# Optimization experiments

Hardware: AMD Instinct MI355X
Metric: run time of the kernel (lower is better)

Reference implementation:

```python
import jax, jax.numpy as jnp
import numpy as np

B, N, D, H = 16, 512, 256, 8
E_PER = 16384  # edges per graph (avg degree 32)
BN_EPS = 1e-5


def _bn(x, g, b, m, v):
    # BatchNorm1d in eval mode: normalize with running stats
    return (x - m) * (g * jax.lax.rsqrt(v + BN_EPS)) + b


def setup_inputs() -> dict:
    key = jax.random.key(0)
    ks = jax.random.split(key, 32)
    E = B * E_PER
    w = lambda k, s: (jax.random.normal(k, s, jnp.float32) * 0.02)
    # block-diagonal edge list: indices within each graph + graph offset
    src = jax.random.randint(ks[1], (B, E_PER), 0, N)
    dst = jax.random.randint(ks[2], (B, E_PER), 0, N)
    off = (jnp.arange(B) * N)[:, None]
    inp = {
        "x": jax.random.normal(ks[0], (B * N, D), jnp.float32),
        "edge_rows": (src + off).reshape(-1).astype(jnp.int32),
        "edge_cols": (dst + off).reshape(-1).astype(jnp.int32),
        "edge_vals": jax.random.uniform(ks[3], (E,), jnp.float32) * 0.1,
        "w_gcn": w(ks[4], (D, D)),
        "in_proj_w": w(ks[5], (3 * D, D)),
        "in_proj_b": w(ks[6], (3 * D,)),
        "out_proj_w": w(ks[7], (D, D)),
        "out_proj_b": w(ks[8], (D,)),
        "w1": w(ks[9], (4 * D, D)),
        "b1": w(ks[10], (4 * D,)),
        "w2": w(ks[11], (D, 4 * D)),
        "b2": w(ks[12], (D,)),
        "batch_size": B,
        "num_nodes": N,
    }
    for i, name in enumerate(["bn1", "bn2", "bn3"]):
        k4 = jax.random.split(ks[13 + i], 4)
        inp[name + "_g"] = 1.0 + jax.random.uniform(k4[0], (D,), jnp.float32) * 0.1
        inp[name + "_b"] = w(k4[1], (D,))
        inp[name + "_m"] = w(k4[2], (D,))
        inp[name + "_v"] = 1.0 + jax.random.uniform(k4[3], (D,), jnp.float32) * 0.1
    return inp


def reference(x, edge_rows, edge_cols, edge_vals, w_gcn,
              in_proj_w, in_proj_b, out_proj_w, out_proj_b,
              bn1_g, bn1_b, bn1_m, bn1_v,
              bn2_g, bn2_b, bn2_m, bn2_v,
              bn3_g, bn3_b, bn3_m, bn3_v,
              w1, b1, w2, b2, batch_size, num_nodes):
    n_total = x.shape[0]
    dh = D // H
    # --- local GCN: linear -> sparse SpMM (gather/scatter) -> exact GELU ---
    hl = x @ w_gcn.T                                            # (BN, D)
    agg = jax.ops.segment_sum(edge_vals[:, None] * hl[edge_cols],
                              edge_rows, num_segments=n_total)   # (BN, D)
    h_local = jax.nn.gelu(agg, approximate=False)
    x = x + h_local
    x = _bn(x, bn1_g, bn1_b, bn1_m, bn1_v)
    # --- global multi-head self-attention per graph ---
    h = x.reshape(batch_size, num_nodes, D)
    qkv = jnp.einsum('bnd,ed->bne', h, in_proj_w) + in_proj_b    # (B, N, 3D)
    q, k, v = jnp.split(qkv, 3, axis=-1)
    q = q.reshape(batch_size, num_nodes, H, dh)
    k = k.reshape(batch_size, num_nodes, H, dh)
    v = v.reshape(batch_size, num_nodes, H, dh)
    scores = jnp.einsum('bqhd,bkhd->bhqk', q, k) / jnp.sqrt(jnp.float32(dh))
    attn = jax.nn.softmax(scores, axis=-1)
    ctx = jnp.einsum('bhqk,bkhd->bqhd', attn, v).reshape(batch_size, num_nodes, D)
    h_attn = (ctx @ out_proj_w.T + out_proj_b).reshape(n_total, D)
    x = x + h_attn
    x = _bn(x, bn2_g, bn2_b, bn2_m, bn2_v)
    # --- FFN ---
    h_ffn = jax.nn.gelu(x @ w1.T + b1, approximate=False) @ w2.T + b2
    x = x + h_ffn
    x = _bn(x, bn3_g, bn3_b, bn3_m, bn3_v)
    return x
```

## Files before the change

kernel.cpp:

```cpp
#include <hip/hip_runtime.h>
#include <hip/hip_bf16.h>
#include <math.h>

#define D_    256
#define NT_   8192
#define NN_   512
#define B_    16
#define H_    8
#define EPG_  16384
#define BN_EPS 1e-5f

typedef __attribute__((ext_vector_type(8))) short bx8;
typedef __attribute__((ext_vector_type(4))) short sx4;
typedef __attribute__((ext_vector_type(4))) float fx4;

__device__ __forceinline__ float gelu_exact(float x) {
    return 0.5f * x * (1.0f + erff(x * 0.70710678118654752f));
}
__device__ __forceinline__ short bf16s(float v) {
    __hip_bfloat16 hb = __float2bfloat16(v);
    return *(short*)&hb;
}

typedef __attribute__((address_space(1))) const unsigned int GU;
typedef __attribute__((address_space(3))) unsigned int LU;
__device__ __forceinline__ void gl_lds16(const void* g, void* l) {
    __builtin_amdgcn_global_load_lds((GU*)g, (LU*)l, 16, 0, 0);
}

template<int TM, int TN, int EPI, int OBF, int RBF>
__global__ __launch_bounds__(256)
void mgemm(const short* __restrict__ A, const short* __restrict__ Bw,
           const float* __restrict__ bias, void* __restrict__ Cout,
           int M, int N, int K,
           long sA, long sB, long sC, long sR,
           const void* __restrict__ resid,
           const float* __restrict__ bng, const float* __restrict__ bnb,
           const float* __restrict__ bnm, const float* __restrict__ bnv)
{
    constexpr int MR = TM / 32, NR = TN / 32;
    constexpr int NIA = TM / 8, NIB = TN / 8;
    __shared__ short As[2][TM][64];
    __shared__ short Bs[2][TN][64];
    const int bz = blockIdx.z;
    A  += (size_t)bz * sA;
    Bw += (size_t)bz * sB;
    const int bm = blockIdx.y * TM, bn = blockIdx.x * TN;
    const int tid = threadIdx.x;
    const int w = tid >> 6, lane = tid & 63;
    const int wm = w >> 1, wn = w & 1;
    const int fr = lane & 15;
    const int srow = lane >> 3;
    const int scol = (((lane & 7) ^ (srow & 7)) << 3);
    fx4 acc[MR][NR] = {};

    auto STAGE = [&](int buf, int k0) {
        #pragma unroll
        for (int i = w; i < NIA + NIB; i += 4) {
            if (i < NIA)
                gl_lds16(A + (size_t)(bm + i * 8 + srow) * K + k0 + scol,
                         (char*)&As[buf][0][0] + i * 1024);
            else
                gl_lds16(Bw + (size_t)(bn + (i - NIA) * 8 + srow) * K + k0 + scol,
                         (char*)&Bs[buf][0][0] + (i - NIA) * 1024);
        }
    };

    STAGE(0, 0);
    __syncthreads();
    const int T = K >> 6;
    for (int t = 0; t < T; ++t) {
        const int cur = t & 1;
        if (t + 1 < T) STAGE(cur ^ 1, (t + 1) << 6);
        #pragma unroll
        for (int ks = 0; ks < 2; ++ks) {
            const int sl = (ks << 2) | (lane >> 4);
            bx8 af[MR], bf[NR];
            #pragma unroll
            for (int m = 0; m < MR; ++m) {
                const int row = wm * (TM / 2) + m * 16 + fr;
                af[m] = *(const bx8*)&As[cur][row][(sl ^ (row & 7)) << 3];
            }
            #pragma unroll
            for (int n = 0; n < NR; ++n) {
                const int row = wn * (TN / 2) + n * 16 + fr;
                bf[n] = *(const bx8*)&Bs[cur][row][(sl ^ (row & 7)) << 3];
            }
            #pragma unroll
            for (int m = 0; m < MR; ++m)
                #pragma unroll
                for (int n = 0; n < NR; ++n)
                    acc[m][n] = __builtin_amdgcn_mfma_f32_16x16x32_bf16(af[m], bf[n], acc[m][n], 0, 0, 0);
        }
        __syncthreads();
    }

    float* Cf = (float*)Cout + (size_t)bz * sC;
    __hip_bfloat16* Cb = (__hip_bfloat16*)Cout + (size_t)bz * sC;
    const float* Rf = (const float*)resid + ((EPI == 2 || EPI == 3) ? (size_t)bz * sR : 0);
    const __hip_bfloat16* Rb = (const __hip_bfloat16*)resid + ((EPI == 2 || EPI == 3) ? (size_t)bz * sR : 0);
    #pragma unroll
    for (int m = 0; m < MR; ++m) {
        #pragma unroll
        for (int n = 0; n < NR; ++n) {
            const int gm0 = bm + wm * (TM / 2) + m * 16 + (lane >> 4) * 4;
            const int gn  = bn + wn * (TN / 2) + n * 16 + fr;
            float vv[4];
            #pragma unroll
            for (int r = 0; r < 4; ++r) {
                const int gm = gm0 + r;
                float v = acc[m][n][r];
                if (bias) v += bias[gn];
                if (EPI == 1) v = gelu_exact(v);
                if (EPI == 2 || EPI == 3) {
                    const float rv = RBF ? __bfloat162float(Rb[(size_t)gm * N + gn])
                                         : Rf[(size_t)gm * N + gn];
                    if (EPI == 2) v += rv;
                    else          v = rv + gelu_exact(v);
                    v = (v - bnm[gn]) * (bng[gn] * rsqrtf(bnv[gn] + BN_EPS)) + bnb[gn];
                }
                vv[r] = v;
            }
            if (EPI == 4) {
                const int tc = (int)sR;
                if (gn >= tc) {
                    short* Tout = (short*)resid;
                    sx4 pk;
                    #pragma unroll
                    for (int r = 0; r < 4; ++r) pk[r] = bf16s(vv[r]);
                    *(sx4*)(Tout + ((size_t)((gm0 >> 9) * (N - tc) + (gn - tc))) * 512 + (gm0 & 511)) = pk;
                } else {
                    #pragma unroll
                    for (int r = 0; r < 4; ++r)
                        Cb[(size_t)(gm0 + r) * N + gn] = __float2bfloat16(vv[r]);
                }
            } else {
                #pragma unroll
                for (int r = 0; r < 4; ++r) {
                    if (OBF) Cb[(size_t)(gm0 + r) * N + gn] = __float2bfloat16(vv[r]);
                    else     Cf[(size_t)(gm0 + r) * N + gn] = vv[r];
                }
            }
        }
    }
}

__device__ __forceinline__ void cv4(const float4 v, __hip_bfloat16* d) {
    __hip_bfloat162* dp = (__hip_bfloat162*)d;
    dp[0] = __hip_bfloat162(__float2bfloat16(v.x), __float2bfloat16(v.y));
    dp[1] = __hip_bfloat162(__float2bfloat16(v.z), __float2bfloat16(v.w));
}

__global__ __launch_bounds__(256)
void conv6(const float* __restrict__ x,  const float* __restrict__ wg,
           const float* __restrict__ iw, const float* __restrict__ ow,
           const float* __restrict__ w1, const float* __restrict__ w2,
           __hip_bfloat16* xb, __hip_bfloat16* wgb, __hip_bfloat16* iwb,
           __hip_bfloat16* owb, __hip_bfloat16* w1b, __hip_bfloat16* w2b)
{
    int i = blockIdx.x * 256 + threadIdx.x;
    const float* s; __hip_bfloat16* d; int o;
    if      (i < 524288) { s = x;  d = xb;  o = i; }
    else if (i < 540672) { s = wg; d = wgb; o = i - 524288; }
    else if (i < 589824) { s = iw; d = iwb; o = i - 540672; }
    else if (i < 606208) { s = ow; d = owb; o = i - 589824; }
    else if (i < 671744) { s = w1; d = w1b; o = i - 606208; }
    else                 { s = w2; d = w2b; o = i - 671744; }
    cv4(((const float4*)s)[o], d + (size_t)o * 4);
}

__global__ __launch_bounds__(256)
void convA(const float* __restrict__ s, __hip_bfloat16* __restrict__ d, int n4)
{
    int i = blockIdx.x * 256 + threadIdx.x;
    if (i >= n4) return;
    cv4(((const float4*)s)[i], d + (size_t)i * 4);
}

__global__ __launch_bounds__(256)
void build_S(const int* __restrict__ rows, const int* __restrict__ cols,
             const float* __restrict__ vals, float* __restrict__ SA)
{
    const int e = blockIdx.x * 256 + threadIdx.x;
    const int r = rows[e], c = cols[e];
    const int g = r >> 9;
    atomicAdd(&SA[((size_t)g << 18) + (size_t)(r & 511) * 512 + (c - (g << 9))], vals[e]);
}

__global__ __launch_bounds__(256, 1)
void attn_mfma(const short* __restrict__ qkv, const short* __restrict__ VtG,
               __hip_bfloat16* __restrict__ ctx)
{
    const int swz = (blockIdx.x & 7) * 128 + (blockIdx.x >> 3);
    const int qt = swz & 7;
    const int h  = (swz >> 3) & 7;
    const int b  = swz >> 6;
    __shared__ short Ks[512][40];
    __shared__ short Vt[32][520];
    __shared__ short Ps[64][520];
    const int tid = threadIdx.x;
    const int lane = tid & 63, wq = tid >> 6;
    const short* base = qkv + (size_t)b * NN_ * 768;
    const short* vtb  = VtG + (size_t)(b * 8 + h) * 32 * 512;

    {
        const int d0 = (tid & 3) << 3;
        const int k0 = tid >> 2;
        #pragma unroll
        for (int rep = 0; rep < 8; ++rep) {
            const int key = k0 + rep * 64;
            *(bx8*)&Ks[key][d0] =
                *(const bx8*)(base + (size_t)key * 768 + 256 + h * 32 + d0);
        }
    }
    {
        const int d = tid >> 3, c0 = (tid & 7) << 3;
        #pragma unroll
        for (int rep = 0; rep < 8; ++rep) {
            const int c = c0 + rep * 64;
            *(bx8*)&Vt[d][c] = *(const bx8*)(vtb + (size_t)d * 512 + c);
        }
    }
    const int fr = lane & 15, fk = (lane >> 4) << 3;
    const int qrow = qt * 64 + wq * 16 + fr;
    bx8 qf = *(const bx8*)(base + (size_t)qrow * 768 + h * 32 + fk);
    __syncthreads();

    fx4 sc[32];
    #pragma unroll
    for (int nt = 0; nt < 32; ++nt) {
        bx8 kf = *(const bx8*)&Ks[nt * 16 + fr][fk];
        fx4 z = {0.f, 0.f, 0.f, 0.f};
        sc[nt] = __builtin_amdgcn_mfma_f32_16x16x32_bf16(kf, qf, z, 0, 0, 0);
    }

    const float scale = 0.17677669529663687f;
    float mx = -1e30f;
    #pragma unroll
    for (int nt = 0; nt < 32; ++nt)
        mx = fmaxf(mx, fmaxf(fmaxf(sc[nt][0], sc[nt][1]), fmaxf(sc[nt][2], sc[nt][3])));
    mx = fmaxf(mx, __shfl_xor(mx, 16, 64));
    mx = fmaxf(mx, __shfl_xor(mx, 32, 64));
    const float M = mx * scale;
    float s = 0.f;
    #pragma unroll
    for (int nt = 0; nt < 32; ++nt) {
        #pragma unroll
        for (int r = 0; r < 4; ++r) {
            const float p = __expf(sc[nt][r] * scale - M);
            sc[nt][r] = p;
            s += p;
        }
    }
    s += __shfl_xor(s, 16, 64);
    s += __shfl_xor(s, 32, 64);
    const float inv = 1.0f / s;
    {
        const int q = wq * 16 + fr;
        const int kb = (lane >> 4) << 2;
        #pragma unroll
        for (int nt = 0; nt < 32; ++nt) {
            sx4 pk;
            #pragma unroll
            for (int r = 0; r < 4; ++r) pk[r] = bf16s(sc[nt][r] * inv);
            *(sx4*)&Ps[q][nt * 16 + kb] = pk;
        }
    }

    fx4 oacc[2] = {};
    #pragma unroll
    for (int step = 0; step < 16; ++step) {
        bx8 pf = *(const bx8*)&Ps[wq * 16 + fr][step * 32 + fk];
        #pragma unroll
        for (int nt = 0; nt < 2; ++nt) {
            bx8 vf = *(const bx8*)&Vt[nt * 16 + fr][step * 32 + fk];
            oacc[nt] = __builtin_amdgcn_mfma_f32_16x16x32_bf16(pf, vf, oacc[nt], 0, 0, 0);
        }
    }
    #pragma unroll
    for (int nt = 0; nt < 2; ++nt) {
        #pragma unroll
        for (int r = 0; r < 4; ++r) {
            const int q = qt * 64 + wq * 16 + (lane >> 4) * 4 + r;
            const int d = nt * 16 + fr;
            ctx[(size_t)(b * NN_ + q) * D_ + h * 32 + d] = __float2bfloat16(oacc[nt][r]);
        }
    }
}

extern "C" void kernel_launch(void* const* d_in, const int* in_sizes, int n_in,
                              void* d_out, int out_size, void* d_ws, size_t ws_size,
                              hipStream_t stream) {
    const float* x      = (const float*)d_in[0];
    const int*   erows  = (const int*)d_in[1];
    const int*   ecols  = (const int*)d_in[2];
    const float* evals  = (const float*)d_in[3];
    const float* w_gcn  = (const float*)d_in[4];
    const float* in_w   = (const float*)d_in[5];
    const float* in_b   = (const float*)d_in[6];
    const float* outw   = (const float*)d_in[7];
    const float* outb   = (const float*)d_in[8];
    const float* w1     = (const float*)d_in[9];
    const float* b1     = (const float*)d_in[10];
    const float* w2     = (const float*)d_in[11];
    const float* b2     = (const float*)d_in[12];
    const float* bn1g = (const float*)d_in[15], *bn1b = (const float*)d_in[16];
    const float* bn1m = (const float*)d_in[17], *bn1v = (const float*)d_in[18];
    const float* bn2g = (const float*)d_in[19], *bn2b = (const float*)d_in[20];
    const float* bn2m = (const float*)d_in[21], *bn2v = (const float*)d_in[22];
    const float* bn3g = (const float*)d_in[23], *bn3b = (const float*)d_in[24];
    const float* bn3m = (const float*)d_in[25], *bn3v = (const float*)d_in[26];

    short* wsS = (short*)d_ws;
    __hip_bfloat16* xb    = (__hip_bfloat16*)(wsS + 0);
    __hip_bfloat16* wgcnb = (__hip_bfloat16*)(wsS + 2097152);
    __hip_bfloat16* iwb   = (__hip_bfloat16*)(wsS + 2162688);
    __hip_bfloat16* owb   = (__hip_bfloat16*)(wsS + 2359296);
    __hip_bfloat16* w1b   = (__hip_bfloat16*)(wsS + 2424832);
    __hip_bfloat16* w2b   = (__hip_bfloat16*)(wsS + 2686976);
    short* VtG  = wsS + 2949120;
    short* hlB  = wsS + 5046272;
    short* x1b  = wsS + 7143424;
    short* ctxb = wsS + 9240576;
    short* x2b  = wsS + 11337728;
    short* h1b  = wsS + 13434880;
    short* SAb  = wsS + 21823488;
    float* SA   = (float*)(wsS + 26017792);
    short* qkvb = wsS + 26017792;
    float* out  = (float*)d_out;

    dim3 blk(256);
    conv6<<<dim3(2880), blk, 0, stream>>>(x, w_gcn, in_w, outw, w1, w2,
                                          xb, wgcnb, iwb, owb, w1b, w2b);
    hipMemsetAsync(SA, 0, (size_t)16 * 512 * 512 * 4, stream);
    build_S<<<dim3(1024), blk, 0, stream>>>(erows, ecols, evals, SA);
    convA<<<dim3(4096), blk, 0, stream>>>(SA, (__hip_bfloat16*)SAb, 1048576);
    mgemm<64,64,4,1,0><<<dim3(4, 128), blk, 0, stream>>>((const short*)xb, (const short*)wgcnb,
        nullptr, nullptr, NT_, D_, D_, 0,0,0,0, hlB, nullptr, nullptr, nullptr, nullptr);
    mgemm<64,64,3,1,0><<<dim3(4, 8, 16), blk, 0, stream>>>(SAb, hlB, nullptr, x1b,
        512, D_, 512, 262144, 131072, 131072, 131072,
        x, bn1g, bn1b, bn1m, bn1v);
    mgemm<64,64,4,1,0><<<dim3(12, 128), blk, 0, stream>>>(x1b, (const short*)iwb, in_b, qkvb,
        NT_, 3 * D_, D_, 0,0,0,512, VtG, nullptr, nullptr, nullptr, nullptr);
    attn_mfma<<<dim3(1024), blk, 0, stream>>>(qkvb, VtG, (__hip_bfloat16*)ctxb);
    mgemm<64,64,2,1,1><<<dim3(4, 128), blk, 0, stream>>>(ctxb, (const short*)owb, outb, x2b,
        NT_, D_, D_, 0,0,0,0, x1b, bn2g, bn2b, bn2m, bn2v);
    mgemm<64,64,1,1,0><<<dim3(16, 128), blk, 0, stream>>>(x2b, (const short*)w1b, b1, h1b,
        NT_, 4 * D_, D_, 0,0,0,0, nullptr, nullptr, nullptr, nullptr, nullptr);
    mgemm<64,64,2,0,1><<<dim3(4, 128), blk, 0, stream>>>(h1b, (const short*)w2b, b2, out,
        NT_, D_, 4 * D_, 0,0,0,0, x2b, bn3g, bn3b, bn3m, bn3v);
}
```

Measured before the change: 230.6 us.

## Stage full 256-wide K chunks in GEMM; read K/V directly from global in attention

The GEMM drops its double-buffered 64-wide K tiles and loads a whole 256-wide K chunk into LDS per step, with a single sync around each chunk. This cuts the number of barriers and loop iterations but gives up overlap between loads and compute and uses more LDS per block. The attention kernel stops copying K and V^T into shared memory and reads the MFMA fragments straight from global memory. That frees LDS so launch bounds can allow 2 blocks per SM, at the cost of uncoalesced, cache-dependent global reads.

```diff
diff --git a/kernel.cpp b/kernel.cpp
--- a/kernel.cpp
+++ b/kernel.cpp
@@ -39,9 +39,9 @@
            const float* __restrict__ bnm, const float* __restrict__ bnv)
 {
     constexpr int MR = TM / 32, NR = TN / 32;
-    constexpr int NIA = TM / 8, NIB = TN / 8;
-    __shared__ short As[2][TM][64];
-    __shared__ short Bs[2][TN][64];
+    constexpr int NIA = TM / 2, NIB = TN / 2;
+    __shared__ short As[TM][256];
+    __shared__ short Bs[TN][256];
     const int bz = blockIdx.z;
     A  += (size_t)bz * sA;
     Bw += (size_t)bz * sB;
@@ -49,42 +49,44 @@
     const int tid = threadIdx.x;
     const int w = tid >> 6, lane = tid & 63;
     const int wm = w >> 1, wn = w & 1;
-    const int fr = lane & 15;
-    const int srow = lane >> 3;
-    const int scol = (((lane & 7) ^ (srow & 7)) << 3);
+    const int fr = lane & 15, hi = lane >> 4;
+    const int rli = lane >> 5;
+    const int sl  = lane & 31;
     fx4 acc[MR][NR] = {};
 
-    auto STAGE = [&](int buf, int k0) {
+    auto STAGE = [&](int kc) {
         #pragma unroll
         for (int i = w; i < NIA + NIB; i += 4) {
-            if (i < NIA)
-                gl_lds16(A + (size_t)(bm + i * 8 + srow) * K + k0 + scol,
-                         (char*)&As[buf][0][0] + i * 1024);
-            else
-                gl_lds16(Bw + (size_t)(bn + (i - NIA) * 8 + srow) * K + k0 + scol,
-                         (char*)&Bs[buf][0][0] + (i - NIA) * 1024);
+            if (i < NIA) {
+                const int row = i * 2 + rli;
+                gl_lds16(A + (size_t)(bm + row) * K + kc + ((sl ^ (row & 7)) << 3),
+                         (char*)As + i * 1024);
+            } else {
+                const int j = i - NIA;
+                const int row = j * 2 + rli;
+                gl_lds16(Bw + (size_t)(bn + row) * K + kc + ((sl ^ (row & 7)) << 3),
+                         (char*)Bs + j * 1024);
+            }
         }
     };
 
-    STAGE(0, 0);
-    __syncthreads();
-    const int T = K >> 6;
-    for (int t = 0; t < T; ++t) {
-        const int cur = t & 1;
-        if (t + 1 < T) STAGE(cur ^ 1, (t + 1) << 6);
-        #pragma unroll
-        for (int ks = 0; ks < 2; ++ks) {
-            const int sl = (ks << 2) | (lane >> 4);
+    const int NC = K >> 8;
+    for (int c = 0; c < NC; ++c) {
+        if (c) __syncthreads();
+        STAGE(c << 8);
+        __syncthreads();
+        #pragma unroll
+        for (int ks = 0; ks < 8; ++ks) {
             bx8 af[MR], bf[NR];
             #pragma unroll
             for (int m = 0; m < MR; ++m) {
                 const int row = wm * (TM / 2) + m * 16 + fr;
-                af[m] = *(const bx8*)&As[cur][row][(sl ^ (row & 7)) << 3];
+                af[m] = *(const bx8*)&As[row][((((ks << 2) | hi) ^ (row & 7)) << 3)];
             }
             #pragma unroll
             for (int n = 0; n < NR; ++n) {
                 const int row = wn * (TN / 2) + n * 16 + fr;
-                bf[n] = *(const bx8*)&Bs[cur][row][(sl ^ (row & 7)) << 3];
+                bf[n] = *(const bx8*)&Bs[row][((((ks << 2) | hi) ^ (row & 7)) << 3)];
             }
             #pragma unroll
             for (int m = 0; m < MR; ++m)
@@ -92,7 +94,6 @@
                 for (int n = 0; n < NR; ++n)
                     acc[m][n] = __builtin_amdgcn_mfma_f32_16x16x32_bf16(af[m], bf[n], acc[m][n], 0, 0, 0);
         }
-        __syncthreads();
     }
 
     float* Cf = (float*)Cout + (size_t)bz * sC;
@@ -103,7 +104,7 @@
     for (int m = 0; m < MR; ++m) {
         #pragma unroll
         for (int n = 0; n < NR; ++n) {
-            const int gm0 = bm + wm * (TM / 2) + m * 16 + (lane >> 4) * 4;
+            const int gm0 = bm + wm * (TM / 2) + m * 16 + hi * 4;
             const int gn  = bn + wn * (TN / 2) + n * 16 + fr;
             float vv[4];
             #pragma unroll
@@ -187,7 +188,7 @@
     atomicAdd(&SA[((size_t)g << 18) + (size_t)(r & 511) * 512 + (c - (g << 9))], vals[e]);
 }
 
-__global__ __launch_bounds__(256, 1)
+__global__ __launch_bounds__(256, 2)
 void attn_mfma(const short* __restrict__ qkv, const short* __restrict__ VtG,
                __hip_bfloat16* __restrict__ ctx)
 {
@@ -195,41 +196,21 @@
     const int qt = swz & 7;
     const int h  = (swz >> 3) & 7;
     const int b  = swz >> 6;
-    __shared__ short Ks[512][40];
-    __shared__ short Vt[32][520];
     __shared__ short Ps[64][520];
     const int tid = threadIdx.x;
     const int lane = tid & 63, wq = tid >> 6;
     const short* base = qkv + (size_t)b * NN_ * 768;
+    const short* kb_  = base + 256 + h * 32;
     const short* vtb  = VtG + (size_t)(b * 8 + h) * 32 * 512;
 
-    {
-        const int d0 = (tid & 3) << 3;
-        const int k0 = tid >> 2;
-        #pragma unroll
-        for (int rep = 0; rep < 8; ++rep) {
-            const int key = k0 + rep * 64;
-            *(bx8*)&Ks[key][d0] =
-                *(const bx8*)(base + (size_t)key * 768 + 256 + h * 32 + d0);
-        }
-    }
-    {
-        const int d = tid >> 3, c0 = (tid & 7) << 3;
-        #pragma unroll
-        for (int rep = 0; rep < 8; ++rep) {
-            const int c = c0 + rep * 64;
-            *(bx8*)&Vt[d][c] = *(const bx8*)(vtb + (size_t)d * 512 + c);
-        }
-    }
-    const int fr = lane & 15, fk = (lane >> 4) << 3;
+    const int fr = lane & 15, hi = lane >> 4, fk = hi << 3;
     const int qrow = qt * 64 + wq * 16 + fr;
     bx8 qf = *(const bx8*)(base + (size_t)qrow * 768 + h * 32 + fk);
-    __syncthreads();
 
     fx4 sc[32];
     #pragma unroll
     for (int nt = 0; nt < 32; ++nt) {
-        bx8 kf = *(const bx8*)&Ks[nt * 16 + fr][fk];
+        bx8 kf = *(const bx8*)(kb_ + (size_t)(nt * 16 + fr) * 768 + fk);
         fx4 z = {0.f, 0.f, 0.f, 0.f};
         sc[nt] = __builtin_amdgcn_mfma_f32_16x16x32_bf16(kf, qf, z, 0, 0, 0);
     }
@@ -257,13 +238,13 @@
     const float inv = 1.0f / s;
     {
         const int q = wq * 16 + fr;
-        const int kb = (lane >> 4) << 2;
+        const int kb2 = hi << 2;
         #pragma unroll
         for (int nt = 0; nt < 32; ++nt) {
             sx4 pk;
             #pragma unroll
             for (int r = 0; r < 4; ++r) pk[r] = bf16s(sc[nt][r] * inv);
-            *(sx4*)&Ps[q][nt * 16 + kb] = pk;
+            *(sx4*)&Ps[q][nt * 16 + kb2] = pk;
         }
     }
 
@@ -273,7 +254,7 @@
         bx8 pf = *(const bx8*)&Ps[wq * 16 + fr][step * 32 + fk];
         #pragma unroll
         for (int nt = 0; nt < 2; ++nt) {
-            bx8 vf = *(const bx8*)&Vt[nt * 16 + fr][step * 32 + fk];
+            bx8 vf = *(const bx8*)(vtb + (size_t)(nt * 16 + fr) * 512 + step * 32 + fk);
             oacc[nt] = __builtin_amdgcn_mfma_f32_16x16x32_bf16(pf, vf, oacc[nt], 0, 0, 0);
         }
     }
@@ -281,7 +262,7 @@
     for (int nt = 0; nt < 2; ++nt) {
         #pragma unroll
         for (int r = 0; r < 4; ++r) {
-            const int q = qt * 64 + wq * 16 + (lane >> 4) * 4 + r;
+            const int q = qt * 64 + wq * 16 + hi * 4 + r;
             const int d = nt * 16 + fr;
             ctx[(size_t)(b * NN_ + q) * D_ + h * 32 + d] = __float2bfloat16(oacc[nt][r]);
         }
```

Measured after the change: 261.8 us. 1.14x slower.
